# Kernel optimization log

Measured on AMD Instinct MI355X. Metric: run time of the kernel, lower is better.

The kernel has to match this reference:

```python
import jax, jax.numpy as jnp
import numpy as np

N = 4096      # total nodes
NPG = 64      # nodes per graph
B = 64        # graphs in batch
D = 256       # d_features
P1 = 32       # pooling size level 1
P2 = 8        # pooling size level 2
E = 65536     # edges
DLIN = 512
DOUT = 256


def setup_inputs() -> dict:
    key = jax.random.key(0)
    ks = jax.random.split(key, 16)
    x = jax.random.normal(ks[0], (N, D), jnp.float32)
    # edges within each graph's contiguous node segment
    base = (jnp.arange(E) % B) * NPG
    src = base + jax.random.randint(ks[1], (E,), 0, NPG)
    dst = base + jax.random.randint(ks[2], (E,), 0, NPG)
    edge_index = jnp.stack([src, dst]).astype(jnp.int32)
    batch = (jnp.arange(N) // NPG).astype(jnp.int32)

    def w(k, i, o):
        return (jax.random.normal(k, (i, o), jnp.float32) / np.sqrt(i)).astype(jnp.float32)

    return {
        "x": x, "edge_index": edge_index, "batch": batch,
        "pool0_W1": w(ks[3], D, D), "pool0_W2": w(ks[4], D, P1),
        "emb0_W1": w(ks[5], D, D), "emb0_W2": w(ks[6], D, D),
        "pool1_W1": w(ks[7], D, D), "pool1_W2": w(ks[8], D, P2),
        "emb1_W1": w(ks[9], D, D), "emb1_W2": w(ks[10], D, D),
        "lin1_W": w(ks[11], D, DLIN), "lin1_b": jnp.zeros((DLIN,), jnp.float32),
        "lin2_W": w(ks[12], DLIN, DOUT), "lin2_b": jnp.zeros((DOUT,), jnp.float32),
    }


def _gnn(X, A, W1, W2):
    # GATEncoder stand-in: two adjacency propagation + linear steps
    H = jax.nn.relu((A @ X + X) @ W1)
    return (A @ H + H) @ W2


def _block_diag(blocks):
    # blocks: (b, s, s) -> dense block-diagonal (b*s, b*s)
    b, s, _ = blocks.shape
    out = jnp.zeros((b, s, b, s), blocks.dtype)
    out = out.at[jnp.arange(b), :, jnp.arange(b), :].set(blocks)
    return out.reshape(b * s, b * s)


def _extract_blocks(A, size, bsz):
    return A.reshape(bsz, size, bsz, size)[jnp.arange(bsz), :, jnp.arange(bsz), :]


def reference(x, edge_index, batch, pool0_W1, pool0_W2, emb0_W1, emb0_W2,
              pool1_W1, pool1_W2, emb1_W1, emb1_W2, lin1_W, lin1_b, lin2_W, lin2_b):
    # dense adjacency scatter-build
    A = jnp.zeros((N, N), x.dtype).at[edge_index[0], edge_index[1]].set(1.0)

    # --- diffpool level 1 (ankward_diffpool; equal-size segments -> batched bmm) ---
    S = jax.nn.softmax(_gnn(x, A, pool0_W1, pool0_W2), axis=-1)   # (N, P1)
    Z = _gnn(x, A, emb0_W1, emb0_W2)                              # (N, D)
    Sb = S.reshape(B, NPG, P1)
    Zb = Z.reshape(B, NPG, D)
    Ab = _extract_blocks(A, NPG, B)                               # (B, NPG, NPG)
    X = jnp.einsum('bns,bnd->bsd', Sb, Zb).reshape(B * P1, D)
    A = _block_diag(jnp.einsum('bns,bnm,bmt->bst', Sb, Ab, Sb))   # (B*P1, B*P1)

    # --- diffpool level 2 (batch_diffpool) ---
    S2 = jax.nn.softmax(_gnn(X, A, pool1_W1, pool1_W2).reshape(B, P1, P2), axis=-1)
    Z2 = _gnn(X, A, emb1_W1, emb1_W2).reshape(B, P1, D)
    Ab2 = _extract_blocks(A, P1, B)                               # (B, P1, P1)
    X = jnp.einsum('bns,bnd->bsd', S2, Z2).reshape(B * P2, D)
    _ = _block_diag(jnp.einsum('bns,bnm,bmt->bst', S2, Ab2, S2))  # built as in original (unused downstream)

    # global mean pool over the regular coarse batch, then final MLP (dropout=eval -> identity)
    Xg = X.reshape(B, P2, D).mean(axis=1)                         # (B, D)
    return jax.nn.relu(Xg @ lin1_W + lin1_b) @ lin2_W + lin2_b    # (B, DOUT)
```

## Files before the change

kernel.cpp:

```cpp
#include <hip/hip_runtime.h>

typedef __attribute__((ext_vector_type(8))) short bfx8;
typedef __attribute__((ext_vector_type(4))) short bfx4;
typedef __attribute__((ext_vector_type(4))) float fx4;
typedef __attribute__((ext_vector_type(4))) int   ix4;

#define OA   0
#define OB0  8192
#define OB1  40960
#define OB2  73728
#define OB3  106496
#define OSP  139264
#define OST  147456
#define OX2  OB1
#define OAS  (OB1+16384)
#define OA2  (OB1+20480)
#define OV   (OB1+22528)
#define OW   (OB1+22656)
#define OU   (OB1+23680)
#define OT1  (OB1+24704)
#define LDS_TOTAL 151552

__device__ __forceinline__ short f2bf(float f){
    union{float f;unsigned u;}v; v.f=f;
    unsigned r = v.u + 0x7FFFu + ((v.u>>16)&1u);
    return (short)(r>>16);
}
__device__ __forceinline__ float bf2f(short s){
    union{unsigned u;float f;}v; v.u = ((unsigned)(unsigned short)s)<<16; return v.f;
}

__device__ __forceinline__ int so16(int r,int c,int pitch){ return ((r*pitch+c)*2) ^ ((r&7)<<4); }
__device__ __forceinline__ int so32(int r,int c,int pitch){ return ((r*pitch+c)*4) ^ ((r&7)<<4); }
__device__ __forceinline__ int mpoff(int r,int c){
    int base = (c&128)? OB2 : OB0;
    return base + so32(r, c&127, 128);
}

__device__ __forceinline__ bfx8 ldfrag(const char* sm,int boff,int r0,int k0,int pitch,int lane){
    int r = r0 + (lane&15);
    int c = k0 + ((lane>>4)<<3);
    return *(const bfx8*)(sm + boff + so16(r,c,pitch));
}

template<int NTL,int KS,int TPW,bool ADD>
__device__ __forceinline__ void gemm_ll_t(const char* sm,int aoff,int ap,int boff,int bp,
                                          int lane,int w,fx4* acc){
#pragma unroll
    for(int i=0;i<TPW;i++){
        int t=w*TPW+i, mt=t>>NTL, nt=t&((1<<NTL)-1);
        fx4 c = ADD? acc[i] : fx4{0.f,0.f,0.f,0.f};
#pragma unroll
        for(int ks=0;ks<KS;ks++){
            bfx8 a = ldfrag(sm,aoff,mt<<4,ks<<5,ap,lane);
            bfx8 b = ldfrag(sm,boff,nt<<4,ks<<5,bp,lane);
            c = __builtin_amdgcn_mfma_f32_16x16x32_bf16(a,b,c,0,0,0);
        }
        acc[i]=c;
    }
}
template<int NTL,int KS,int TPW,bool ADD>
__device__ __forceinline__ void gemm_lg_t(const char* sm,int aoff,int ap,const bfx8* pk,
                                          int lane,int w,fx4* acc){
#pragma unroll
    for(int i=0;i<TPW;i++){
        int t=w*TPW+i, mt=t>>NTL, nt=t&((1<<NTL)-1);
        fx4 c = ADD? acc[i] : fx4{0.f,0.f,0.f,0.f};
#pragma unroll
        for(int ks=0;ks<KS;ks++){
            bfx8 a = ldfrag(sm,aoff,mt<<4,ks<<5,ap,lane);
            bfx8 b = pk[(nt*KS+ks)*64 + lane];
            c = __builtin_amdgcn_mfma_f32_16x16x32_bf16(a,b,c,0,0,0);
        }
        acc[i]=c;
    }
}

template<int NTL,int TPW>
__device__ __forceinline__ void st_norm(char* sm,int boff,int pitch,int lane,int w,
                                        const fx4* acc,bool relu){
#pragma unroll
    for(int i=0;i<TPW;i++){
        int t=w*TPW+i, mt=t>>NTL, nt=t&((1<<NTL)-1);
        int col=(nt<<4)+(lane&15), rb=(mt<<4)+((lane>>4)<<2);
#pragma unroll
        for(int q=0;q<4;q++){
            float v=acc[i][q]; if(relu) v=fmaxf(v,0.f);
            *(short*)(sm+boff+so16(rb+q,col,pitch)) = f2bf(v);
        }
    }
}
template<int NTL,int TPW>
__device__ __forceinline__ void st_norm_hilo(char* sm,int bhi,int blo,int pitch,int lane,int w,
                                             const fx4* acc,bool relu){
#pragma unroll
    for(int i=0;i<TPW;i++){
        int t=w*TPW+i, mt=t>>NTL, nt=t&((1<<NTL)-1);
        int col=(nt<<4)+(lane&15), rb=(mt<<4)+((lane>>4)<<2);
#pragma unroll
        for(int q=0;q<4;q++){
            float v=acc[i][q]; if(relu) v=fmaxf(v,0.f);
            short hi=f2bf(v);
            *(short*)(sm+bhi+so16(rb+q,col,pitch)) = hi;
            *(short*)(sm+blo+so16(rb+q,col,pitch)) = f2bf(v - bf2f(hi));
        }
    }
}
template<int NTL,int TPW>
__device__ __forceinline__ void st_tr(char* sm,int boff,int pitch,int lane,int w,
                                      const fx4* acc,bool relu){
#pragma unroll
    for(int i=0;i<TPW;i++){
        int t=w*TPW+i, mt=t>>NTL, nt=t&((1<<NTL)-1);
        int rn=(nt<<4)+(lane&15), cb=(mt<<4)+((lane>>4)<<2);
        bfx4 p;
#pragma unroll
        for(int q=0;q<4;q++){ float v=acc[i][q]; if(relu) v=fmaxf(v,0.f); p[q]=f2bf(v); }
        *(bfx4*)(sm+boff+so16(rn,cb,pitch)) = p;
    }
}
template<int NTL,int TPW>
__device__ __forceinline__ void st_tr_hilo(char* sm,int bhi,int blo,int pitch,int lane,int w,
                                           const fx4* acc,bool relu){
#pragma unroll
    for(int i=0;i<TPW;i++){
        int t=w*TPW+i, mt=t>>NTL, nt=t&((1<<NTL)-1);
        int rn=(nt<<4)+(lane&15), cb=(mt<<4)+((lane>>4)<<2);
        bfx4 ph, pl;
#pragma unroll
        for(int q=0;q<4;q++){
            float v=acc[i][q]; if(relu) v=fmaxf(v,0.f);
            short hi=f2bf(v); ph[q]=hi; pl[q]=f2bf(v - bf2f(hi));
        }
        *(bfx4*)(sm+bhi+so16(rn,cb,pitch)) = ph;
        *(bfx4*)(sm+blo+so16(rn,cb,pitch)) = pl;
    }
}
template<int TPW>
__device__ __forceinline__ void st_mp(char* sm,int lane,int w,const fx4* acc){
#pragma unroll
    for(int i=0;i<TPW;i++){
        int t=w*TPW+i, mt=t>>4, nt=t&15;
        int col=(nt<<4)+(lane&15), rb=(mt<<4)+((lane>>4)<<2);
#pragma unroll
        for(int q=0;q<4;q++) *(float*)(sm+mpoff(rb+q,col)) = acc[i][q];
    }
}

__global__ __launch_bounds__(256) void prepack_k(const float* __restrict__ Wp1,const float* __restrict__ We1,
                                                 const float* __restrict__ We2,const float* __restrict__ We21,
                                                 short* __restrict__ outp){
    int g = blockIdx.x; int seg = g>>5;
    int t = ((g&31)<<8) + threadIdx.x;
    int lane = t&63, tile = t>>6, kt = tile&7, nt = tile>>3;
    const float* W = (seg<2)? Wp1 : (seg==2)? We1 : (seg==3)? We2 : We21;
    int kb  = (kt<<5) + ((lane>>4)<<3);
    int col = (nt<<4) + (lane&15);
    bfx8 o;
#pragma unroll
    for(int j=0;j<8;j++){
        float v = W[(kb+j)*256 + col];
        short hi = f2bf(v);
        o[j] = (seg==1)? f2bf(v - bf2f(hi)) : hi;
    }
    ((bfx8*)outp)[seg*8192 + t] = o;
}

__global__ __launch_bounds__(1024) void mega_k(const float* __restrict__ x, const int* __restrict__ ei,
        const float* __restrict__ Wp2,  const float* __restrict__ We22,
        const float* __restrict__ l1W,  const float* __restrict__ l1b,
        const float* __restrict__ l2W,  const float* __restrict__ l2b,
        const short* __restrict__ pks,  float* __restrict__ out){
    extern __shared__ char sm[];
    const int tid = threadIdx.x, lane = tid&63, w = tid>>6, b = blockIdx.x;
    const bfx8* pkWp1hi = (const bfx8*)pks;
    const bfx8* pkWp1lo = pkWp1hi + 8192;
    const bfx8* pkWe1   = pkWp1hi + 16384;
    const bfx8* pkWe2   = pkWp1hi + 24576;
    const bfx8* pkWe21  = pkWp1hi + 32768;
    fx4 acc[4];

    if(tid<512) *(ix4*)(sm + OA + tid*16) = ix4{0,0,0,0};
#pragma unroll
    for(int ch=0; ch<4; ch++){
        int i2 = tid + (ch<<10);
        int r = i2>>6, c0 = (i2&63)<<2;
        fx4 v = *(const fx4*)(x + (size_t)(((b<<6)+r)<<8) + c0);
#pragma unroll
        for(int j=0;j<4;j++)
            *(short*)(sm + OB0 + so16(c0+j, r, 64)) = f2bf(v[j]);
    }
    __syncthreads();
    {
        int e = b + (tid<<6);
        int s = ei[e]&63, d = ei[e+65536]&63;
        *(short*)(sm + OA + so16(s, d, 64)) = (short)0x3F80;
    }
    __syncthreads();
    if(tid<64){
        int off = OA + so16(tid, tid, 64);
        *(short*)(sm+off) = f2bf(bf2f(*(short*)(sm+off)) + 1.0f);
    }
    __syncthreads();

    gemm_ll_t<4,2,4,false>(sm, OA,64, OB0,64, lane,w, acc);
    st_norm_hilo<4,4>(sm, OB1, OB2, 256, lane,w, acc, false);
    __syncthreads();

    gemm_lg_t<4,8,4,false>(sm, OB1,256, pkWe1, lane,w, acc);
    st_tr<4,4>(sm, OB3, 64, lane,w, acc, true);
    gemm_lg_t<4,8,4,false>(sm, OB1,256, pkWp1hi, lane,w, acc);
    gemm_lg_t<4,8,4,true >(sm, OB1,256, pkWp1lo, lane,w, acc);
    gemm_lg_t<4,8,4,true >(sm, OB2,256, pkWp1hi, lane,w, acc);
    __syncthreads();
    st_tr_hilo<4,4>(sm, OB0, OB2, 64, lane,w, acc, true);
    __syncthreads();

    gemm_ll_t<4,2,4,false>(sm, OA,64, OB0,64, lane,w, acc);
    gemm_ll_t<4,2,4,true >(sm, OA,64, OB2,64, lane,w, acc);
    __syncthreads();
    st_mp<4>(sm, lane,w, acc);
    __syncthreads();

    if(tid<512){
        int r = tid>>3, sg = tid&7;
        float a0=0.f,a1=0.f,a2=0.f,a3=0.f;
        for(int c=0;c<256;c++){
            float m = *(const float*)(sm + mpoff(r,c));
            fx4 wv = *(const fx4*)(Wp2 + (c<<5) + (sg<<2));
            a0 += m*wv[0]; a1 += m*wv[1]; a2 += m*wv[2]; a3 += m*wv[3];
        }
        *(float*)(sm+OSP+so32(r,(sg<<2)+0,32))=a0;
        *(float*)(sm+OSP+so32(r,(sg<<2)+1,32))=a1;
        *(float*)(sm+OSP+so32(r,(sg<<2)+2,32))=a2;
        *(float*)(sm+OSP+so32(r,(sg<<2)+3,32))=a3;
    }
    __syncthreads();
    if(tid<512){
        int r = tid>>3, j = tid&7;
        float v0=*(const float*)(sm+OSP+so32(r,(j<<2)+0,32));
        float v1=*(const float*)(sm+OSP+so32(r,(j<<2)+1,32));
        float v2=*(const float*)(sm+OSP+so32(r,(j<<2)+2,32));
        float v3=*(const float*)(sm+OSP+so32(r,(j<<2)+3,32));
        float mx = fmaxf(fmaxf(v0,v1),fmaxf(v2,v3));
#pragma unroll
        for(int o=1;o<8;o<<=1) mx = fmaxf(mx, __shfl_xor(mx,o,64));
        float e0=__expf(v0-mx), e1=__expf(v1-mx), e2=__expf(v2-mx), e3=__expf(v3-mx);
        float s = e0+e1+e2+e3;
#pragma unroll
        for(int o=1;o<8;o<<=1) s += __shfl_xor(s,o,64);
        float inv = 1.f/s;
        *(short*)(sm+OST+so16((j<<2)+0,r,64)) = f2bf(e0*inv);
        *(short*)(sm+OST+so16((j<<2)+1,r,64)) = f2bf(e1*inv);
        *(short*)(sm+OST+so16((j<<2)+2,r,64)) = f2bf(e2*inv);
        *(short*)(sm+OST+so16((j<<2)+3,r,64)) = f2bf(e3*inv);
    }
    __syncthreads();

    gemm_ll_t<4,2,4,false>(sm, OA,64, OB3,64, lane,w, acc);
    st_norm<4,4>(sm, OB1, 256, lane,w, acc, false);
    __syncthreads();
    gemm_lg_t<4,8,4,false>(sm, OB1,256, pkWe2, lane,w, acc);
    st_tr<4,4>(sm, OB2, 64, lane,w, acc, false);
    __syncthreads();
    gemm_ll_t<4,2,2,false>(sm, OST,64, OB2,64, lane,w, acc);
    st_tr<4,2>(sm, OX2, 32, lane,w, acc, false);
    __syncthreads();
    if(w<8){
        gemm_ll_t<1,2,1,false>(sm, OA,64, OST,64, lane,w, acc);
        int mt = w>>1, nt = w&1;
        int tcol = (nt<<4)+(lane&15), cb = (mt<<4)+((lane>>4)<<2);
        bfx4 p;
#pragma unroll
        for(int q=0;q<4;q++){
            float v = acc[0][q] - bf2f(*(const short*)(sm+OST+so16(tcol,cb+q,64)));
            p[q]=f2bf(v);
        }
        *(bfx4*)(sm+OAS+so16(tcol,cb,64)) = p;
    }
    __syncthreads();
    if(w<4){
        gemm_ll_t<1,2,1,false>(sm, OST,64, OAS,64, lane,w, acc);
        int mt=w>>1, nt=w&1;
        int col=(nt<<4)+(lane&15), rb=(mt<<4)+((lane>>4)<<2);
#pragma unroll
        for(int q=0;q<4;q++){
            float v = acc[0][q] + ((rb+q)==col ? 1.f : 0.f);
            *(short*)(sm+OA2+so16(rb+q,col,32)) = f2bf(v);
        }
    }
    __syncthreads();
    if(tid<32){
        float s=0.f;
#pragma unroll
        for(int r=0;r<32;r++) s += bf2f(*(const short*)(sm+OA2+so16(r,tid,32)));
        *(float*)(sm+OV+(tid<<2)) = s;
    }
    __syncthreads();
    gemm_ll_t<4,1,2,false>(sm, OA2,32, OX2,32, lane,w, acc);
    st_norm<4,2>(sm, OB3, 256, lane,w, acc, false);
    __syncthreads();
    gemm_lg_t<4,8,2,false>(sm, OB3,256, pkWe21, lane,w, acc);
    st_norm<4,2>(sm, OB0, 256, lane,w, acc, true);
    __syncthreads();
    if(tid<256){
        float a=0.f;
#pragma unroll
        for(int n=0;n<32;n++)
            a += *(const float*)(sm+OV+(n<<2)) * bf2f(*(const short*)(sm+OB0+so16(n,tid,256)));
        *(float*)(sm+OW+(tid<<2)) = a;
    }
    __syncthreads();
    if(tid<256){
        float a=0.f;
        for(int k=0;k<256;k++) a += *(const float*)(sm+OW+(k<<2)) * We22[(k<<8)+tid];
        *(float*)(sm+OU+(tid<<2)) = 0.125f*a;
    }
    __syncthreads();
    if(tid<512){
        float a = l1b[tid];
        for(int k=0;k<256;k++) a += *(const float*)(sm+OU+(k<<2)) * l1W[(k<<9)+tid];
        *(float*)(sm+OT1+(tid<<2)) = fmaxf(a,0.f);
    }
    __syncthreads();
    if(tid<256){
        float a = l2b[tid];
        for(int k=0;k<512;k++) a += *(const float*)(sm+OT1+(k<<2)) * l2W[(k<<8)+tid];
        out[(b<<8)+tid] = a;
    }
}

extern "C" void kernel_launch(void* const* d_in, const int* in_sizes, int n_in,
                              void* d_out, int out_size, void* d_ws, size_t ws_size,
                              hipStream_t stream) {
    const float* x    = (const float*)d_in[0];
    const int*   ei   = (const int*)d_in[1];
    const float* p0W1 = (const float*)d_in[3];
    const float* p0W2 = (const float*)d_in[4];
    const float* e0W1 = (const float*)d_in[5];
    const float* e0W2 = (const float*)d_in[6];
    const float* e1W1 = (const float*)d_in[9];
    const float* e1W2 = (const float*)d_in[10];
    const float* l1W  = (const float*)d_in[11];
    const float* l1b  = (const float*)d_in[12];
    const float* l2W  = (const float*)d_in[13];
    const float* l2b  = (const float*)d_in[14];
    float* out = (float*)d_out;
    short* pks = (short*)d_ws;

    hipFuncSetAttribute((const void*)mega_k, hipFuncAttributeMaxDynamicSharedMemorySize, LDS_TOTAL);
    prepack_k<<<160, 256, 0, stream>>>(p0W1, e0W1, e0W2, e1W1, pks);
    mega_k<<<64, 1024, LDS_TOTAL, stream>>>(x, ei, p0W2, e1W2, l1W, l1b, l2W, l2b, pks, out);
}
```

Baseline: 193.8 us.

## Reorder MFMA loops, add sched barriers, widen Wp2 projection, unroll tail GEMVs

The MFMA helper loops are interchanged so the k-step is outermost and several independent accumulator tiles are issued back to back, hiding MFMA dependency latency. Scheduling barriers are placed between the chained pooling GEMMs, and the launch bounds now request a minimum waves-per-EU hint. The Wp2 projection is spread over all 1024 threads with two outputs each instead of 512 threads with four, and the final GEMV loops get unroll pragmas. These trade register pressure and scheduling freedom for more instruction-level parallelism in a single-block-per-graph mega kernel.

```diff
diff --git a/kernel.cpp b/kernel.cpp
--- a/kernel.cpp
+++ b/kernel.cpp
@@ -3,6 +3,7 @@
 typedef __attribute__((ext_vector_type(8))) short bfx8;
 typedef __attribute__((ext_vector_type(4))) short bfx4;
 typedef __attribute__((ext_vector_type(4))) float fx4;
+typedef __attribute__((ext_vector_type(2))) float fx2;
 typedef __attribute__((ext_vector_type(4))) int   ix4;
 
 #define OA   0
@@ -46,33 +47,37 @@
 template<int NTL,int KS,int TPW,bool ADD>
 __device__ __forceinline__ void gemm_ll_t(const char* sm,int aoff,int ap,int boff,int bp,
                                           int lane,int w,fx4* acc){
-#pragma unroll
-    for(int i=0;i<TPW;i++){
-        int t=w*TPW+i, mt=t>>NTL, nt=t&((1<<NTL)-1);
-        fx4 c = ADD? acc[i] : fx4{0.f,0.f,0.f,0.f};
-#pragma unroll
-        for(int ks=0;ks<KS;ks++){
+    if(!ADD){
+#pragma unroll
+        for(int i=0;i<TPW;i++) acc[i]=fx4{0.f,0.f,0.f,0.f};
+    }
+#pragma unroll
+    for(int ks=0;ks<KS;ks++){
+#pragma unroll
+        for(int i=0;i<TPW;i++){
+            int t=w*TPW+i, mt=t>>NTL, nt=t&((1<<NTL)-1);
             bfx8 a = ldfrag(sm,aoff,mt<<4,ks<<5,ap,lane);
             bfx8 b = ldfrag(sm,boff,nt<<4,ks<<5,bp,lane);
-            c = __builtin_amdgcn_mfma_f32_16x16x32_bf16(a,b,c,0,0,0);
-        }
-        acc[i]=c;
+            acc[i] = __builtin_amdgcn_mfma_f32_16x16x32_bf16(a,b,acc[i],0,0,0);
+        }
     }
 }
 template<int NTL,int KS,int TPW,bool ADD>
 __device__ __forceinline__ void gemm_lg_t(const char* sm,int aoff,int ap,const bfx8* pk,
                                           int lane,int w,fx4* acc){
-#pragma unroll
-    for(int i=0;i<TPW;i++){
-        int t=w*TPW+i, mt=t>>NTL, nt=t&((1<<NTL)-1);
-        fx4 c = ADD? acc[i] : fx4{0.f,0.f,0.f,0.f};
-#pragma unroll
-        for(int ks=0;ks<KS;ks++){
+    if(!ADD){
+#pragma unroll
+        for(int i=0;i<TPW;i++) acc[i]=fx4{0.f,0.f,0.f,0.f};
+    }
+#pragma unroll 2
+    for(int ks=0;ks<KS;ks++){
+#pragma unroll
+        for(int i=0;i<TPW;i++){
+            int t=w*TPW+i, mt=t>>NTL, nt=t&((1<<NTL)-1);
             bfx8 a = ldfrag(sm,aoff,mt<<4,ks<<5,ap,lane);
             bfx8 b = pk[(nt*KS+ks)*64 + lane];
-            c = __builtin_amdgcn_mfma_f32_16x16x32_bf16(a,b,c,0,0,0);
-        }
-        acc[i]=c;
+            acc[i] = __builtin_amdgcn_mfma_f32_16x16x32_bf16(a,b,acc[i],0,0,0);
+        }
     }
 }
 
@@ -166,7 +171,7 @@
     ((bfx8*)outp)[seg*8192 + t] = o;
 }
 
-__global__ __launch_bounds__(1024) void mega_k(const float* __restrict__ x, const int* __restrict__ ei,
+__global__ __launch_bounds__(1024, 4) void mega_k(const float* __restrict__ x, const int* __restrict__ ei,
         const float* __restrict__ Wp2,  const float* __restrict__ We22,
         const float* __restrict__ l1W,  const float* __restrict__ l1b,
         const float* __restrict__ l2W,  const float* __restrict__ l2b,
@@ -209,8 +214,11 @@
 
     gemm_lg_t<4,8,4,false>(sm, OB1,256, pkWe1, lane,w, acc);
     st_tr<4,4>(sm, OB3, 64, lane,w, acc, true);
+    __builtin_amdgcn_sched_barrier(0);
     gemm_lg_t<4,8,4,false>(sm, OB1,256, pkWp1hi, lane,w, acc);
+    __builtin_amdgcn_sched_barrier(0);
     gemm_lg_t<4,8,4,true >(sm, OB1,256, pkWp1lo, lane,w, acc);
+    __builtin_amdgcn_sched_barrier(0);
     gemm_lg_t<4,8,4,true >(sm, OB2,256, pkWp1hi, lane,w, acc);
     __syncthreads();
     st_tr_hilo<4,4>(sm, OB0, OB2, 64, lane,w, acc, true);
@@ -222,18 +230,16 @@
     st_mp<4>(sm, lane,w, acc);
     __syncthreads();
 
-    if(tid<512){
-        int r = tid>>3, sg = tid&7;
-        float a0=0.f,a1=0.f,a2=0.f,a3=0.f;
+    {
+        int r = tid>>4, j = tid&15;
+        float a0=0.f,a1=0.f;
+#pragma unroll 4
         for(int c=0;c<256;c++){
             float m = *(const float*)(sm + mpoff(r,c));
-            fx4 wv = *(const fx4*)(Wp2 + (c<<5) + (sg<<2));
-            a0 += m*wv[0]; a1 += m*wv[1]; a2 += m*wv[2]; a3 += m*wv[3];
-        }
-        *(float*)(sm+OSP+so32(r,(sg<<2)+0,32))=a0;
-        *(float*)(sm+OSP+so32(r,(sg<<2)+1,32))=a1;
-        *(float*)(sm+OSP+so32(r,(sg<<2)+2,32))=a2;
-        *(float*)(sm+OSP+so32(r,(sg<<2)+3,32))=a3;
+            fx2 wv = *(const fx2*)(Wp2 + (c<<5) + (j<<1));
+            a0 += m*wv[0]; a1 += m*wv[1];
+        }
+        *(fx2*)(sm+OSP+so32(r,(j<<1),32)) = fx2{a0,a1};
     }
     __syncthreads();
     if(tid<512){
@@ -313,18 +319,21 @@
     __syncthreads();
     if(tid<256){
         float a=0.f;
+#pragma unroll 8
         for(int k=0;k<256;k++) a += *(const float*)(sm+OW+(k<<2)) * We22[(k<<8)+tid];
         *(float*)(sm+OU+(tid<<2)) = 0.125f*a;
     }
     __syncthreads();
     if(tid<512){
         float a = l1b[tid];
+#pragma unroll 8
         for(int k=0;k<256;k++) a += *(const float*)(sm+OU+(k<<2)) * l1W[(k<<9)+tid];
         *(float*)(sm+OT1+(tid<<2)) = fmaxf(a,0.f);
     }
     __syncthreads();
     if(tid<256){
         float a = l2b[tid];
+#pragma unroll 8
         for(int k=0;k<512;k++) a += *(const float*)(sm+OT1+(k<<2)) * l2W[(k<<8)+tid];
         out[(b<<8)+tid] = a;
     }
```

Result: no change. 197.6 us (+2.0%).
